# Performance work log

Hardware: AMD Instinct MI355X
Metric: run time of the kernel (lower is better)

The kernel has to match this reference:

```python
import math
import jax, jax.numpy as jnp
import numpy as np
from jax import lax

jax.config.update("jax_enable_x64", True)

DECOMP_LEVEL = 5
# Daubechies-5 (db5) decomposition low-pass filter (pywt convention)
_DB5_LO = np.array([0.003335725285001549, -0.012580751999015526, -0.006241490213011705,
                    0.07757149384006515, -0.03224486958502952, -0.24229488706619015,
                    0.13842814590110342, 0.7243085284385744, 0.6038292697974729,
                    0.160102397974125], dtype=np.float64)
_L = _DB5_LO.size
_DB5_HI = _DB5_LO[::-1].copy() * ((-1.0) ** np.arange(_L))  # QMF high-pass
LO = jnp.asarray(_DB5_LO, jnp.float32)
HI = jnp.asarray(_DB5_HI, jnp.float32)
LOR = jnp.asarray(_DB5_LO[::-1].copy(), jnp.float32)
HIR = jnp.asarray(_DB5_HI[::-1].copy(), jnp.float32)


def _an_last(x):
    # orthonormal periodized analysis along last axis: (..., n) -> (..., n/2) x2
    n = x.shape[-1]
    lead = x.shape[:-1]
    xp = jnp.concatenate([x, x[..., : _L - 2]], axis=-1).reshape(-1, 1, n + _L - 2)
    k = jnp.stack([LO, HI])[:, None, :]  # (2,1,L)
    y = lax.conv_general_dilated(xp, k, (2,), "VALID")  # (B,2,n/2)
    y = y.reshape(lead + (2, n // 2))
    return y[..., 0, :], y[..., 1, :]


def _syn_last(a, d):
    # exact transpose/inverse of _an_last (orthonormal -> W^T = W^-1)
    n2 = a.shape[-1]
    n = 2 * n2
    lead = a.shape[:-1]
    B = int(np.prod(lead)) if lead else 1
    u = jnp.zeros((B, 2, n), a.dtype)
    u = u.at[:, 0, ::2].set(a.reshape(B, n2))
    u = u.at[:, 1, ::2].set(d.reshape(B, n2))
    up = jnp.concatenate([u[..., -(_L - 1):], u], axis=-1)  # circular left pad
    k = jnp.stack([LOR, HIR])[None, :, :]  # (1,2,L)
    y = lax.conv_general_dilated(up, k, (1,), "VALID")  # (B,1,n)
    return y.reshape(lead + (n,))


def _dwt2(x):  # x: (C,h,w) -> ll, lh, hl, hh each (C,h/2,w/2)
    a_h, d_h = _an_last(x.swapaxes(-1, -2))
    a_h = a_h.swapaxes(-1, -2)
    d_h = d_h.swapaxes(-1, -2)
    ll, lh = _an_last(a_h)
    hl, hh = _an_last(d_h)
    return ll, lh, hl, hh


def _idwt2(ll, lh, hl, hh):
    a_h = _syn_last(ll, lh)
    d_h = _syn_last(hl, hh)
    return _syn_last(a_h.swapaxes(-1, -2), d_h.swapaxes(-1, -2)).swapaxes(-1, -2)


def _estimate_noise(data):
    p = data.shape[0]
    rr = data @ data.T
    rri = jnp.linalg.inv(rr + 1e-6 * jnp.eye(p, dtype=data.dtype))
    def per_band(i):
        xx = rri - jnp.outer(rri[:, i], rri[i, :]) / rri[i, i]
        beta = xx @ rr[:, i]
        return beta.at[i].set(0.0)
    betas = jax.vmap(per_band)(jnp.arange(p))  # (p,p)
    return data - betas @ data


def hyres_forward(x):
    H, W, K = x.shape
    N = H * W
    data = x.reshape(N, K).T.astype(jnp.float64)
    w = _estimate_noise(data)
    omega1 = (jnp.sqrt(jnp.var(w, axis=1, ddof=1)) + 1e-30) ** 2  # (K,) f64
    y_w = x * omega1 ** -0.5  # whitened, f64
    u, s, v_pca = jnp.linalg.svd(y_w.reshape(N, K), full_matrices=False)
    pc = (u * s).reshape(W, H, K).astype(jnp.float32).transpose(2, 0, 1)  # (K,H,W)
    # multi-level 2D DWT per channel
    ll = pc
    highs = []
    for _ in range(DECOMP_LEVEL):
        ll, lh, hl, hh = _dwt2(ll)
        highs.append((lh, hl, hh))
    # overwrite-style full coefficient image [[LL,LH],[HL,HH]] recursively
    full = ll
    for lh, hl, hh in reversed(highs):
        top = jnp.concatenate([full, lh], axis=-1)
        bot = jnp.concatenate([hl, hh], axis=-1)
        full = jnp.concatenate([top, bot], axis=-2)
    V = full.transpose(1, 2, 0).reshape(N, K)
    V2 = V * V
    norm_v = jnp.sum(V2)
    n_xyz = jnp.asarray(V.size, jnp.float32)
    col_norm = jnp.sum(V2, axis=0)  # (K,)
    # SURE of soft-threshold over a 15-point grid in [0, sqrt(log N)]
    ts = np.linspace(0.0, math.sqrt(math.log(N)), 15).astype(np.float32)
    sure_cols = []
    for t in ts:
        t2 = float(t * t)
        s_t = (jnp.sum(jnp.minimum(V2, t2), axis=0)
               + 2.0 * jnp.sum((V2 > t2).astype(jnp.float32), axis=0)
               - col_norm)
        sure_cols.append(s_t)
    sure_all = jnp.stack(sure_cols, axis=1)  # (K,15)
    c_const = norm_v - n_xyz
    # replicate the in-place cumulative update: S_r = sum_{j<r} S_j + sure_r + C
    def step(acc, sure_r):
        s_r = acc + sure_r + c_const
        return acc + s_r, jnp.min(s_r)
    _, min_sure = lax.scan(step, jnp.zeros((15,), jnp.float32), sure_all)
    # early-exit: first rank>1 where min_sure increases; else loop ends at K-1
    cond = min_sure[2:] > min_sure[1:-1]
    rank = jnp.where(jnp.any(cond), 2 + jnp.argmax(cond), K - 1)
    mask = (jnp.arange(K) < rank).astype(jnp.float32)[:, None, None]
    # truncation-to-rank == zeroing channels >= rank (inverse DWT is linear)
    y = ll * mask
    for lh, hl, hh in reversed(highs):
        y = _idwt2(y, lh * mask, hl * mask, hh * mask)
    y_est = y.transpose(1, 2, 0).reshape(N, K)  # zero cols beyond rank
    out = (omega1.astype(jnp.float32) ** 0.5) * (y_est @ v_pca.astype(jnp.float32)).reshape(H, W, K)
    return out


def setup_inputs() -> dict:
    key = jax.random.key(0)
    k1, k2, k3 = jax.random.split(key, 3)
    H = W = 384
    K = 191
    R = 8  # low-rank spectral structure + noise, as HyRes assumes
    a = jax.random.normal(k1, (H * W, R), jnp.float32)
    b = jax.random.normal(k2, (R, K), jnp.float32)
    x = (a @ b) / np.sqrt(R) + 0.1 * jax.random.normal(k3, (H * W, K), jnp.float32)
    return {"x": x.reshape(H, W, K)}


def reference(x):
    return hyres_forward(x)
```

## Files before the change

### kernel.cpp

```cpp
#include <hip/hip_runtime.h>
#include <math.h>

#define K_     191
#define LD     192
#define N_     147456
#define MSUB   16
#define NT     15
#define TRI_N  18336
#define SMEM_CHOL  ((TRI_N + 1056 + 64) * 8)
#define SMEM_SOLVE ((TRI_N + 192 + 192 + 192) * 8)
#define SMEM2_SZ (6880 * 8 + 32 * 4 + TRI_N * 4)

#define NPAIR  6
#define NSPLIT 256
#define CHUNK  (N_ / NSPLIT)
#define RSTEP  16

__constant__ float c_lo[10] = {
  0.003335725285001549f, -0.012580751999015526f, -0.006241490213011705f,
  0.07757149384006515f,  -0.03224486958502952f, -0.24229488706619015f,
  0.13842814590110342f,   0.7243085284385744f,   0.6038292697974729f,
  0.160102397974125f };
__constant__ float c_hi[10] = {
  0.160102397974125f,    -0.6038292697974729f,   0.7243085284385744f,
 -0.13842814590110342f,  -0.24229488706619015f,  0.03224486958502952f,
  0.07757149384006515f,   0.006241490213011705f,-0.012580751999015526f,
 -0.003335725285001549f };

__global__ __launch_bounds__(256, 6) void k_rr(const float* __restrict__ x,
                                               double* __restrict__ rrg,
                                               double* __restrict__ m)
{
  __shared__ float Asf[2][RSTEP][64];
  __shared__ float Bsf[2][RSTEP][64];

  const int bid   = blockIdx.x;
  const int split = bid & (NSPLIT - 1);
  const int pair  = bid >> 8;
  const int BI[6] = {0, 0, 0, 1, 1, 2};
  const int BJ[6] = {0, 1, 2, 1, 2, 2};
  const int bi = BI[pair], bj = BJ[pair];
  const int diag = (bi == bj);
  const int ca = bi * 64, cb = bj * 64;

  const int t  = threadIdx.x;
  const int tx = t & 15, ty = t >> 4;
  const int mycol = t & 63, rowgrp = t >> 6;
  const long n0 = (long)split * CHUNK;

  double acc[4][4];
  #pragma unroll
  for (int v = 0; v < 4; ++v)
    #pragma unroll
    for (int u = 0; u < 4; ++u) acc[v][u] = 0.0;
  double csum = 0.0;

  float ra[4], rbv[4];
  const int cA = ca + mycol, cB = cb + mycol;
  const bool okA = (cA < K_), okB = (cB < K_);

  auto LOADT = [&](int r0) {
    #pragma unroll
    for (int i = 0; i < 4; ++i) {
      int row = i * 4 + rowgrp;
      long gr = (n0 + r0 + row) * (long)K_;
      float va = okA ? x[gr + cA] : 0.f;
      ra[i] = va;
      if (diag) csum += (double)va;
      else      rbv[i] = okB ? x[gr + cB] : 0.f;
    }
  };
  auto WRITET = [&](int buf) {
    #pragma unroll
    for (int i = 0; i < 4; ++i) {
      int row = i * 4 + rowgrp;
      Asf[buf][row][mycol] = ra[i];
      if (!diag) Bsf[buf][row][mycol] = rbv[i];
    }
  };

  LOADT(0);
  WRITET(0);
  __syncthreads();

  int cur = 0;
  for (int r0 = 0; r0 < CHUNK; r0 += RSTEP) {
    const bool hasnext = (r0 + RSTEP < CHUNK);
    if (hasnext) LOADT(r0 + RSTEP);
    const float (*As)[64] = Asf[cur];
    const float (*Bs)[64] = diag ? Asf[cur] : Bsf[cur];
    #pragma unroll 4
    for (int k = 0; k < RSTEP; ++k) {
      double a0 = (double)As[k][ty],      a1 = (double)As[k][ty + 16];
      double a2 = (double)As[k][ty + 32], a3 = (double)As[k][ty + 48];
      double b0 = (double)Bs[k][tx],      b1 = (double)Bs[k][tx + 16];
      double b2 = (double)Bs[k][tx + 32], b3 = (double)Bs[k][tx + 48];
      acc[0][0] += a0 * b0; acc[0][1] += a0 * b1; acc[0][2] += a0 * b2; acc[0][3] += a0 * b3;
      acc[1][0] += a1 * b0; acc[1][1] += a1 * b1; acc[1][2] += a1 * b2; acc[1][3] += a1 * b3;
      acc[2][0] += a2 * b0; acc[2][1] += a2 * b1; acc[2][2] += a2 * b2; acc[2][3] += a2 * b3;
      acc[3][0] += a3 * b0; acc[3][1] += a3 * b1; acc[3][2] += a3 * b2; acc[3][3] += a3 * b3;
    }
    if (hasnext) WRITET(cur ^ 1);
    __syncthreads();
    cur ^= 1;
  }

  #pragma unroll
  for (int v = 0; v < 4; ++v) {
    int mrow = ca + ty + 16 * v;
    #pragma unroll
    for (int u = 0; u < 4; ++u) {
      int ncol = cb + tx + 16 * u;
      if (mrow < K_ && ncol < K_ && (!diag || mrow <= ncol))
        atomicAdd(&rrg[(size_t)mrow * K_ + ncol], acc[v][u]);
    }
  }

  if (diag) {
    double* sc = (double*)Bsf;
    sc[t] = csum;
    __syncthreads();
    if (t < 64) {
      int c = ca + t;
      if (c < K_) {
        double s = sc[t] + sc[t + 64] + sc[t + 128] + sc[t + 192];
        atomicAdd(&m[c], s);
      }
    }
  }
}

__global__ __launch_bounds__(256) void k_reduce(const double* __restrict__ rrg,
                                                double* __restrict__ rr)
{
  int idx = blockIdx.x * 256 + threadIdx.x;
  if (idx >= TRI_N) return;
  int i = (int)((sqrtf(8.f * (float)idx + 1.f) - 1.f) * 0.5f);
  while ((i + 1) * (i + 2) / 2 <= idx) ++i;
  while (i * (i + 1) / 2 > idx) --i;
  int j = idx - (i * (i + 1)) / 2;
  double s = rrg[(size_t)j * K_ + i];
  rr[i * LD + j] = s;
  rr[j * LD + i] = s;
}

__global__ __launch_bounds__(512) void k_chol(
    const double* __restrict__ rr, double* __restrict__ Lg,
    double* __restrict__ rdg)
{
  extern __shared__ double smem[];
  double* tri  = smem;
  double* tmp  = smem + TRI_N;
  double* tmp2 = tmp + 1056;
  const int t = threadIdx.x;

  for (int i = t >> 5; i < K_; i += 16) {
    int base = (i * (i + 1)) / 2;
    for (int j = t & 31; j <= i; j += 32) {
      double v = rr[i * LD + j];
      tri[base + j] = (i == j) ? v + 1e-6 : v;
    }
  }
  __syncthreads();

  for (int J = 0; J < 6; ++J) {
    const int j0 = J * 32;
    const int nb = (K_ - j0 < 32) ? (K_ - j0) : 32;

    if (t < 64) {
      const int rl = t & 31;
      double a[32];
      #pragma unroll
      for (int c = 0; c < 32; ++c) {
        int i = j0 + rl;
        a[c] = (c <= rl && rl < nb) ? tri[(i * (i + 1)) / 2 + j0 + c] : 0.0;
      }
      #pragma unroll
      for (int k = 0; k < 32; ++k) {
        double akk = __shfl(a[k], k);
        double piv = sqrt(akk);
        double inv = 1.0 / piv;
        if (t == k) {
          tmp2[k] = inv;
          if (j0 + k < K_) rdg[j0 + k] = inv;
        }
        a[k] = (rl == k) ? piv : a[k] * inv;
        #pragma unroll
        for (int c = k + 1; c < 32; ++c) {
          double lck = __shfl(a[k], c);
          if (c <= rl) a[c] -= a[k] * lck;
        }
      }
      if (t < 32 && rl < nb) {
        int i = j0 + rl;
        int rb = (i * (i + 1)) / 2 + j0;
        #pragma unroll
        for (int c = 0; c < 32; ++c)
          if (c <= rl) tri[rb + c] = a[c];
      }
    }
    if (t < 32) {
      const int c = t;
      double xcol[32];
      #pragma unroll
      for (int r = 0; r < 32; ++r) {
        int rr_ = (j0 + r < K_) ? j0 + r : K_ - 1;
        int rb2 = (rr_ * (rr_ + 1)) / 2 + j0;
        double s = (r == c) ? 1.0 : 0.0;
        #pragma unroll
        for (int k = 0; k < 32; ++k)
          if (k < r) s -= tri[rb2 + k] * xcol[k];
        xcol[r] = s * tmp2[r];
      }
      #pragma unroll
      for (int r = 0; r < 32; ++r)
        tmp[r * 33 + c] = (r >= c) ? xcol[r] : 0.0;
    }
    __syncthreads();

    {
      int p = j0 + 32 + t;
      if (nb == 32 && p < K_) {
        int pb = (p * (p + 1)) / 2 + j0;
        double arow[32];
        #pragma unroll
        for (int k = 0; k < 32; ++k) arow[k] = tri[pb + k];
        #pragma unroll
        for (int c = 0; c < 32; ++c) {
          double s = 0.0;
          #pragma unroll
          for (int k = 0; k < 32; ++k)
            if (k <= c) s += arow[k] * tmp[c * 33 + k];
          tri[pb + c] = s;
        }
      }
    }
    __syncthreads();

    {
      int s0 = j0 + 32;
      int n = K_ - s0;
      if (n > 0) {
        int R4 = (n + 3) >> 2;
        int T4 = R4 * (R4 + 1) / 2;
        for (int tile = t; tile < T4; tile += 512) {
          int ti = (int)((sqrtf(8.f * (float)tile + 1.f) - 1.f) * 0.5f);
          while ((ti + 1) * (ti + 2) / 2 <= tile) ++ti;
          while (ti * (ti + 1) / 2 > tile) --ti;
          int tj = tile - ti * (ti + 1) / 2;
          int r0 = s0 + ti * 4, c0 = s0 + tj * 4;
          int rb[4], cb[4];
          #pragma unroll
          for (int u = 0; u < 4; ++u) {
            int r = (r0 + u < K_) ? r0 + u : K_ - 1;
            rb[u] = (r * (r + 1)) / 2;
            int c = (c0 + u < K_) ? c0 + u : K_ - 1;
            cb[u] = (c * (c + 1)) / 2;
          }
          double acc[4][4];
          #pragma unroll
          for (int u = 0; u < 4; ++u)
            #pragma unroll
            for (int v2 = 0; v2 < 4; ++v2) acc[u][v2] = 0.0;
          #pragma unroll 4
          for (int p = 0; p < 32; ++p) {
            double lr[4], lc[4];
            #pragma unroll
            for (int u = 0; u < 4; ++u) {
              lr[u] = tri[rb[u] + j0 + p];
              lc[u] = tri[cb[u] + j0 + p];
            }
            #pragma unroll
            for (int u = 0; u < 4; ++u)
              #pragma unroll
              for (int v2 = 0; v2 < 4; ++v2) acc[u][v2] += lr[u] * lc[v2];
          }
          #pragma unroll
          for (int u = 0; u < 4; ++u) {
            int r = r0 + u;
            if (r < K_) {
              #pragma unroll
              for (int v2 = 0; v2 < 4; ++v2) {
                int c = c0 + v2;
                if (c <= r) tri[rb[u] + c] -= acc[u][v2];
              }
            }
          }
        }
      }
    }
    __syncthreads();
  }

  for (int idx = t; idx < TRI_N; idx += 512) Lg[idx] = tri[idx];
}

__global__ __launch_bounds__(256) void k_csolve(
    const double* __restrict__ Lg, const double* __restrict__ rdg,
    const double* __restrict__ mg, double* __restrict__ s2g,
    double* __restrict__ zg)
{
  extern __shared__ double ssm[];
  double* Ls   = ssm;
  double* rd_s = Ls + TRI_N;
  double* m_sh = rd_s + 192;
  double* ys   = m_sh + 192;
  const int t = threadIdx.x;
  const int bid = blockIdx.x;

  const int start = (bid < K_) ? (bid * (bid + 1)) / 2 : 0;
  for (int idx = start + t; idx < TRI_N; idx += 256) Ls[idx] = Lg[idx];
  if (t < K_) { rd_s[t] = rdg[t]; m_sh[t] = mg[t]; }
  __syncthreads();

  if (t >= 64) return;
  const int l = t;

  if (bid < K_) {
    const int i = bid;
    double x0 = 0.0, x1 = 0.0, x2 = 0.0;
    {
      double rdi = rd_s[i];
      if ((i & 63) == l) {
        int sl = i >> 6;
        if (sl == 0) x0 = rdi; else if (sl == 1) x1 = rdi; else x2 = rdi;
      }
    }
    for (int r = i + 1; r < K_; ++r) {
      int rb = (r * (r + 1)) >> 1;
      double partial = 0.0;
      { int k = l;       if (k < r) partial += Ls[rb + k] * x0; }
      { int k = l + 64;  if (k < r) partial += Ls[rb + k] * x1; }
      { int k = l + 128; if (k < r) partial += Ls[rb + k] * x2; }
      #pragma unroll
      for (int mm = 32; mm > 0; mm >>= 1) partial += __shfl_xor(partial, mm);
      double val = -partial * rd_s[r];
      if ((r & 63) == l) {
        int sl = r >> 6;
        if (sl == 0) x0 = val; else if (sl == 1) x1 = val; else x2 = val;
      }
    }
    double s2p = x0 * x0 + x1 * x1 + x2 * x2;
    #pragma unroll
    for (int mm = 32; mm > 0; mm >>= 1) s2p += __shfl_xor(s2p, mm);
    if (l == 0) s2g[i] = s2p;
  } else {
    double y0 = 0.0, y1 = 0.0, y2 = 0.0;
    for (int r = 0; r < K_; ++r) {
      int rb = (r * (r + 1)) >> 1;
      double partial = 0.0;
      { int k = l;       if (k < r) partial += Ls[rb + k] * y0; }
      { int k = l + 64;  if (k < r) partial += Ls[rb + k] * y1; }
      { int k = l + 128; if (k < r) partial += Ls[rb + k] * y2; }
      #pragma unroll
      for (int mm = 32; mm > 0; mm >>= 1) partial += __shfl_xor(partial, mm);
      double val = (m_sh[r] - partial) * rd_s[r];
      if ((r & 63) == l) {
        int sl = r >> 6;
        if (sl == 0) y0 = val; else if (sl == 1) y1 = val; else y2 = val;
      }
      if (l == 0) ys[r] = val;
    }
    double z0 = 0.0, z1 = 0.0, z2 = 0.0;
    for (int r = K_ - 1; r >= 0; --r) {
      double partial = 0.0;
      { int k = l;       if (k > r && k < K_) partial += Ls[((k * (k + 1)) >> 1) + r] * z0; }
      { int k = l + 64;  if (k > r && k < K_) partial += Ls[((k * (k + 1)) >> 1) + r] * z1; }
      { int k = l + 128; if (k > r && k < K_) partial += Ls[((k * (k + 1)) >> 1) + r] * z2; }
      #pragma unroll
      for (int mm = 32; mm > 0; mm >>= 1) partial += __shfl_xor(partial, mm);
      double val = (ys[r] - partial) * rd_s[r];
      if ((r & 63) == l) {
        int sl = r >> 6;
        if (sl == 0) z0 = val; else if (sl == 1) z1 = val; else z2 = val;
      }
      if (l == 0) zg[r] = val;
    }
  }
}

__global__ __launch_bounds__(256) void k_finals(
    const double* __restrict__ rr, const double* __restrict__ s2g,
    const double* __restrict__ zg, double* __restrict__ invsq,
    float* __restrict__ normv)
{
  __shared__ double tmps[K_];
  const int t = threadIdx.x;
  if (t < K_) {
    double dii = s2g[t];
    double q = 1.0 / dii;
    double sm_ = zg[t] / dii;
    double var = (q - sm_ * sm_ / (double)N_) / (double)(N_ - 1);
    double t1 = sqrt(var) + 1e-30;
    double om = t1 * t1;
    invsq[t] = 1.0 / sqrt(om);
    tmps[t] = rr[t * LD + t] / om;
  }
  __syncthreads();
  if (t < 64) {
    double s = 0.0;
    for (int i = t; i < K_; i += 64) s += tmps[i];
    #pragma unroll
    for (int off = 32; off > 0; off >>= 1) s += __shfl_down(s, off);
    if (t == 0) *normv = (float)s;
  }
}

__device__ __forceinline__ void cholqr(double* shQ, double* shS, int t)
{
  if (t < MSUB * MSUB) {
    int a = t & (MSUB - 1), b = t >> 4;
    double s = 0.0;
    for (int r = 0; r < K_; ++r) s += shQ[r * MSUB + a] * shQ[r * MSUB + b];
    shS[b * 17 + a] = s;
  }
  __syncthreads();
  for (int k = 0; k < MSUB; ++k) {
    if (t == 0) shS[k * 17 + k] = sqrt(shS[k * 17 + k]);
    __syncthreads();
    if (t > k && t < MSUB) shS[t * 17 + k] /= shS[k * 17 + k];
    __syncthreads();
    if (t < MSUB * MSUB) {
      int r = t & (MSUB - 1), c = t >> 4;
      if (c > k && r >= c) shS[r * 17 + c] -= shS[r * 17 + k] * shS[c * 17 + k];
    }
    __syncthreads();
  }
  if (t < K_) {
    double q[MSUB];
    #pragma unroll
    for (int c = 0; c < MSUB; ++c) {
      double v = shQ[t * MSUB + c];
      for (int p = 0; p < c; ++p) v -= q[p] * shS[c * 17 + p];
      q[c] = v / shS[c * 17 + c];
    }
    #pragma unroll
    for (int c = 0; c < MSUB; ++c) shQ[t * MSUB + c] = q[c];
  }
  __syncthreads();
}

__global__ __launch_bounds__(512) void k_sub(
    const double* __restrict__ rr, const double* __restrict__ invsq,
    float* __restrict__ W1, float* __restrict__ W2)
{
  extern __shared__ double dsm[];
  double* shQ  = dsm;
  double* shZ  = shQ + 3056;
  double* shS  = shZ + 3056;
  double* Ws   = shS + 272;
  double* inv_s= Ws + 272;
  double* ev   = inv_s + 192;
  double* cs_  = ev + 16;
  double* sn_  = cs_ + 8;
  int* ipp  = (int*)(sn_ + 8);
  int* iqq  = ipp + 8;
  int* perm = iqq + 8;
  float* tri = (float*)(perm + 16);
  const int t = threadIdx.x;

  if (t < K_) inv_s[t] = invsq[t];
  __syncthreads();
  for (int i = t >> 4; i < K_; i += 32) {
    int base = (i * (i + 1)) / 2;
    double di = inv_s[i];
    for (int j = t & 15; j <= i; j += 16)
      tri[base + j] = (float)(rr[i * LD + j] * di * inv_s[j]);
  }
  __syncthreads();

  for (int idx = t; idx < K_ * MSUB; idx += 512) {
    int i = idx >> 4, c = idx & 15;
    float g = (i >= c) ? tri[(i * (i + 1)) / 2 + c] : tri[(c * (c + 1)) / 2 + i];
    shQ[idx] = (double)g;
  }
  __syncthreads();

  cholqr(shQ, shS, t);
  for (int it = 0; it < 4; ++it) {
    for (int idx = t; idx < K_ * MSUB; idx += 512) shZ[idx] = shQ[idx];
    __syncthreads();
    if (t < 96 * 4) {
      int i2 = t >> 2, c4 = t & 3;
      int r0 = 2 * i2, r1 = r0 + 1;
      int has1 = (r1 < K_);
      int rb0 = (r0 * (r0 + 1)) >> 1;
      int rb1 = has1 ? ((r1 * (r1 + 1)) >> 1) : rb0;
      int cb0 = c4 * 4;
      double s0a = 0.0, s0b = 0.0, s0c = 0.0, s0d = 0.0;
      double s1a = 0.0, s1b = 0.0, s1c = 0.0, s1d = 0.0;
      #pragma unroll 2
      for (int k = 0; k <= r0; ++k) {
        double g0 = (double)tri[rb0 + k];
        double g1 = (double)tri[rb1 + k];
        double za = shZ[k * MSUB + cb0],     zb = shZ[k * MSUB + cb0 + 1];
        double zc = shZ[k * MSUB + cb0 + 2], zd = shZ[k * MSUB + cb0 + 3];
        s0a += g0 * za; s0b += g0 * zb; s0c += g0 * zc; s0d += g0 * zd;
        s1a += g1 * za; s1b += g1 * zb; s1c += g1 * zc; s1d += g1 * zd;
      }
      if (has1) {
        double g0 = (double)tri[rb1 + r0];
        double g1 = (double)tri[rb1 + r1];
        double za = shZ[r1 * MSUB + cb0],     zb = shZ[r1 * MSUB + cb0 + 1];
        double zc = shZ[r1 * MSUB + cb0 + 2], zd = shZ[r1 * MSUB + cb0 + 3];
        s0a += g0 * za; s0b += g0 * zb; s0c += g0 * zc; s0d += g0 * zd;
        s1a += g1 * za; s1b += g1 * zb; s1c += g1 * zc; s1d += g1 * zd;
      }
      int kk = ((r1 + 1) * (r1 + 2)) >> 1;
      #pragma unroll 2
      for (int k = r1 + 1; k < K_; ++k) {
        double g0 = (double)tri[kk + r0];
        double g1 = (double)tri[kk + r1];
        double za = shZ[k * MSUB + cb0],     zb = shZ[k * MSUB + cb0 + 1];
        double zc = shZ[k * MSUB + cb0 + 2], zd = shZ[k * MSUB + cb0 + 3];
        s0a += g0 * za; s0b += g0 * zb; s0c += g0 * zc; s0d += g0 * zd;
        s1a += g1 * za; s1b += g1 * zb; s1c += g1 * zc; s1d += g1 * zd;
        kk += k + 1;
      }
      shQ[r0 * MSUB + cb0]     = s0a;
      shQ[r0 * MSUB + cb0 + 1] = s0b;
      shQ[r0 * MSUB + cb0 + 2] = s0c;
      shQ[r0 * MSUB + cb0 + 3] = s0d;
      if (has1) {
        shQ[r1 * MSUB + cb0]     = s1a;
        shQ[r1 * MSUB + cb0 + 1] = s1b;
        shQ[r1 * MSUB + cb0 + 2] = s1c;
        shQ[r1 * MSUB + cb0 + 3] = s1d;
      }
    }
    __syncthreads();
    if (it < 3) cholqr(shQ, shS, t);
  }
  if (t < MSUB * MSUB) {
    int a = t & 15, b = t >> 4;
    double s = 0.0;
    for (int r = 0; r < K_; ++r) s += shZ[r * MSUB + b] * shQ[r * MSUB + a];
    shS[b * 17 + a] = s;
  }
  if (t < MSUB * 17) Ws[t] = 0.0;
  __syncthreads();
  if (t < MSUB) Ws[t * 17 + t] = 1.0;
  __syncthreads();
  for (int sweep = 0; sweep < 6; ++sweep) {
    for (int round = 0; round < 15; ++round) {
      if (t < 8) {
        int ia = (t == 0) ? 0 : (1 + ((t - 1 + round) % 15));
        int ib = 1 + ((14 - t + round) % 15);
        int p = ia < ib ? ia : ib;
        int q = ia < ib ? ib : ia;
        double app = shS[p * 17 + p], aqq = shS[q * 17 + q], apq = shS[p * 17 + q];
        double c = 1.0, s = 0.0;
        if (fabs(apq) > 1e-30 * (fabs(app) + fabs(aqq)) && apq != 0.0) {
          double tau = (aqq - app) / (2.0 * apq);
          double tt = (tau >= 0.0 ? 1.0 : -1.0) / (fabs(tau) + sqrt(1.0 + tau * tau));
          c = 1.0 / sqrt(1.0 + tt * tt); s = tt * c;
        }
        cs_[t] = c; sn_[t] = s; ipp[t] = p; iqq[t] = q;
      }
      __syncthreads();
      if (t < 128) {
        int i = t & 15, mI = t >> 4;
        int p = ipp[mI], q = iqq[mI];
        double c = cs_[mI], s = sn_[mI];
        double u = shS[i * 17 + p], v = shS[i * 17 + q];
        shS[i * 17 + p] = c * u - s * v; shS[i * 17 + q] = s * u + c * v;
        double wu = Ws[i * 17 + p], wv = Ws[i * 17 + q];
        Ws[i * 17 + p] = c * wu - s * wv; Ws[i * 17 + q] = s * wu + c * wv;
      }
      __syncthreads();
      if (t < 128) {
        int j = t & 15, mI = t >> 4;
        int p = ipp[mI], q = iqq[mI];
        double c = cs_[mI], s = sn_[mI];
        double u = shS[p * 17 + j], v = shS[q * 17 + j];
        shS[p * 17 + j] = c * u - s * v; shS[q * 17 + j] = s * u + c * v;
      }
      __syncthreads();
    }
  }
  if (t == 0) {
    for (int i = 0; i < MSUB; ++i) { ev[i] = shS[i * 17 + i]; perm[i] = i; }
    for (int i = 0; i < MSUB; ++i) {
      int best = i;
      for (int j = i + 1; j < MSUB; ++j)
        if (ev[perm[j]] > ev[perm[best]]) best = j;
      int tp = perm[i]; perm[i] = perm[best]; perm[best] = tp;
    }
  }
  __syncthreads();
  for (int idx = t; idx < K_ * MSUB; idx += 512) {
    int i = idx >> 4, c = idx & 15;
    int pc_ = perm[c];
    double e = 0.0;
    #pragma unroll
    for (int p = 0; p < MSUB; ++p) e += shZ[i * MSUB + p] * Ws[p * 17 + pc_];
    W1[i * MSUB + c] = (float)(inv_s[i] * e);
    W2[c * K_ + i]   = (float)(e / inv_s[i]);
  }
}

__global__ __launch_bounds__(256) void k_pc(const float* __restrict__ x,
                                            const float* __restrict__ W1,
                                            float* __restrict__ pc)
{
  __shared__ float xs[32][192];
  __shared__ float w1s[K_ * MSUB];
  int t = threadIdx.x;
  long n0 = (long)blockIdx.x * 32;
  for (int idx = t; idx < K_ * MSUB; idx += 256) w1s[idx] = W1[idx];
  for (int idx = t; idx < 32 * K_; idx += 256) {
    int row = idx / K_, col = idx - row * K_;
    xs[row][col] = x[(n0 + row) * K_ + col];
  }
  __syncthreads();
  int c = t & 15, nl = t >> 4;
  float a0 = 0.f, a1 = 0.f;
  for (int k = 0; k < K_; ++k) {
    float w = w1s[k * MSUB + c];
    a0 += xs[nl][k] * w;
    a1 += xs[nl + 16][k] * w;
  }
  __syncthreads();
  float* ts = &xs[0][0];
  ts[c * 33 + nl]      = a0;
  ts[c * 33 + nl + 16] = a1;
  __syncthreads();
  for (int idx = t; idx < MSUB * 32; idx += 256) {
    int cc = idx >> 5, nn = idx & 31;
    pc[(size_t)cc * N_ + n0 + nn] = ts[cc * 33 + nn];
  }
}

__global__ __launch_bounds__(256) void k_dwt2(const float* __restrict__ in,
                                              float* __restrict__ llout,
                                              float* __restrict__ coef,
                                              int s, long offL, int last,
                                              int ntr)
{
  __shared__ float xin[40][41];
  __shared__ float las[16][41];
  __shared__ float lds_[16][41];
  const int h = s >> 1;
  const int t = threadIdx.x;
  int bid = blockIdx.x;
  int ch = bid / (ntr * ntr);
  int rem = bid - ch * (ntr * ntr);
  int tr = rem / ntr, tc = rem - tr * ntr;
  int rv0 = tr * 16, mc0 = tc * 16;
  const float* cin = in + (long)ch * s * s;

  for (int idx = t; idx < 40 * 40; idx += 256) {
    int i = idx / 40, c = idx - i * 40;
    int gr = (2 * rv0 + i) % s;
    int gc = (2 * mc0 + c) % s;
    xin[i][c] = cin[(long)gr * s + gc];
  }
  __syncthreads();

  for (int idx = t; idx < 16 * 40; idx += 256) {
    int i = idx / 40, c = idx - i * 40;
    float la = 0.f, ld = 0.f;
    #pragma unroll
    for (int l = 0; l < 10; ++l) {
      float v = xin[2 * i + l][c];
      la += c_lo[l] * v; ld += c_hi[l] * v;
    }
    las[i][c] = la; lds_[i][c] = ld;
  }
  __syncthreads();

  {
    int i = t >> 4, j = t & 15;
    int rv = rv0 + i, mc = mc0 + j;
    if (rv < h && mc < h) {
      float ll = 0.f, lh = 0.f, hl = 0.f, hh = 0.f;
      #pragma unroll
      for (int l = 0; l < 10; ++l) {
        float a = las[i][2 * j + l];
        float d = lds_[i][2 * j + l];
        ll += c_lo[l] * a; lh += c_hi[l] * a;
        hl += c_lo[l] * d; hh += c_hi[l] * d;
      }
      float* cslab = coef + (size_t)ch * N_ + offL;
      llout[(size_t)ch * h * h + (long)rv * h + mc] = ll;
      if (last) coef[(size_t)ch * N_ + 147312 + (long)rv * h + mc] = ll;
      cslab[(long)rv * h + mc] = lh;
      cslab[(long)h * h + (long)rv * h + mc] = hl;
      cslab[(long)2 * h * h + (long)rv * h + mc] = hh;
    }
  }
}

__global__ __launch_bounds__(256) void k_stats(const float* __restrict__ coef,
                                               float* __restrict__ stats)
{
  int ch = blockIdx.x;
  int t = threadIdx.x;
  float T2[NT];
  {
    double stop = sqrt(log(147456.0));
    double step = stop / 14.0;
    for (int i = 0; i < NT; ++i) {
      double td = (i == 14) ? stop : (double)i * step;
      float tf = (float)td;
      T2[i] = tf * tf;
    }
  }
  float cn = 0.f, sm[NT], ct[NT];
  #pragma unroll
  for (int i = 0; i < NT; ++i) { sm[i] = 0.f; ct[i] = 0.f; }
  const float* base = coef + (size_t)ch * N_;
  for (int idx = t; idx < N_; idx += 256) {
    float v = base[idx];
    float v2 = v * v;
    cn += v2;
    #pragma unroll
    for (int i = 0; i < NT; ++i) {
      sm[i] += fminf(v2, T2[i]);
      ct[i] += (v2 > T2[i]) ? 1.0f : 0.0f;
    }
  }
  __shared__ float red2[4][32];
  int lane = t & 63, wv = t >> 6;
  for (int a = 0; a < 31; ++a) {
    float val = (a == 0) ? cn : ((a < 16) ? sm[a - 1] : ct[a - 16]);
    #pragma unroll
    for (int off = 32; off > 0; off >>= 1) val += __shfl_down(val, off);
    if (lane == 0) red2[wv][a] = val;
  }
  __syncthreads();
  if (t < 31)
    stats[ch * 31 + t] = red2[0][t] + red2[1][t] + red2[2][t] + red2[3][t];
}

__global__ void k_rank(const float* __restrict__ stats,
                       const float* __restrict__ normv, int* __restrict__ rankp)
{
  if (threadIdx.x != 0 || blockIdx.x != 0) return;
  float c_const = *normv - 28164096.0f;
  float acc[NT];
  for (int i = 0; i < NT; ++i) acc[i] = 0.f;
  float minsure[MSUB];
  for (int r = 0; r < MSUB; ++r) {
    float cn = stats[r * 31 + 0];
    float mn = 3.4e38f;
    for (int i = 0; i < NT; ++i) {
      float sure = stats[r * 31 + 1 + i] + 2.0f * stats[r * 31 + 16 + i] - cn;
      float s_r = acc[i] + sure + c_const;
      acc[i] = acc[i] + s_r;
      if (s_r < mn) mn = s_r;
    }
    minsure[r] = mn;
  }
  int rank = -1;
  for (int r = 2; r < MSUB; ++r) {
    if (minsure[r] > minsure[r - 1]) { rank = r; break; }
  }
  if (rank < 0) rank = MSUB - 1;
  *rankp = rank;
}

__global__ __launch_bounds__(256) void k_out(const float* __restrict__ pc,
                                             const float* __restrict__ W2,
                                             const int* __restrict__ rankp,
                                             float* __restrict__ out)
{
  long gid = (long)blockIdx.x * 256 + threadIdx.x;
  int n = (int)(gid / K_);
  int j = (int)(gid - (long)n * K_);
  int rank = *rankp;
  float acc = 0.f;
  for (int c = 0; c < rank; ++c)
    acc += pc[(size_t)c * N_ + n] * W2[c * K_ + j];
  out[gid] = acc;
}

extern "C" void kernel_launch(void* const* d_in, const int* in_sizes, int n_in,
                              void* d_out, int out_size, void* d_ws, size_t ws_size,
                              hipStream_t stream)
{
  if (n_in < 1 || in_sizes[0] != N_ * K_) return;
  const float* x = (const float*)d_in[0];
  float* out = (float*)d_out;
  (void)out_size;

  char* w = (char*)d_ws;
  size_t off = 0;
  auto alloc = [&](size_t bytes) -> char* {
    char* p = w + off;
    off = (off + bytes + 255) & ~(size_t)255;
    return p;
  };
  double* m_    = (double*)alloc(K_ * 8);
  double* rrp   = (double*)alloc((size_t)K_ * K_ * 8);
  double* rr    = (double*)alloc((size_t)K_ * LD * 8);
  double* Lg    = (double*)alloc((size_t)TRI_N * 8);
  double* rdg   = (double*)alloc(192 * 8);
  double* s2g   = (double*)alloc(192 * 8);
  double* zg    = (double*)alloc(192 * 8);
  double* invsq = (double*)alloc(K_ * 8);
  float*  normv = (float*)alloc(256);
  float*  W1    = (float*)alloc((size_t)K_ * MSUB * 4);
  float*  W2    = (float*)alloc((size_t)MSUB * K_ * 4);
  float*  pc    = (float*)alloc((size_t)MSUB * N_ * 4);
  float*  coef  = (float*)alloc((size_t)MSUB * N_ * 4);
  float*  curA  = (float*)alloc((size_t)MSUB * 192 * 192 * 4);
  float*  curB  = (float*)alloc((size_t)MSUB * 96 * 96 * 4);
  float*  stats = (float*)alloc((size_t)MSUB * 31 * 4);
  int*    rankp = (int*)alloc(256);
  if (off > ws_size) return;

  hipMemsetAsync(m_, 0, K_ * sizeof(double), stream);
  hipMemsetAsync(rrp, 0, (size_t)K_ * K_ * sizeof(double), stream);

  hipFuncSetAttribute(reinterpret_cast<const void*>(k_chol),
                      hipFuncAttributeMaxDynamicSharedMemorySize, SMEM_CHOL);
  hipFuncSetAttribute(reinterpret_cast<const void*>(k_csolve),
                      hipFuncAttributeMaxDynamicSharedMemorySize, SMEM_SOLVE);
  hipFuncSetAttribute(reinterpret_cast<const void*>(k_sub),
                      hipFuncAttributeMaxDynamicSharedMemorySize, SMEM2_SZ);

  k_rr<<<NPAIR * NSPLIT, 256, 0, stream>>>(x, rrp, m_);
  k_reduce<<<(TRI_N + 255) / 256, 256, 0, stream>>>(rrp, rr);
  k_chol<<<1, 512, SMEM_CHOL, stream>>>(rr, Lg, rdg);
  k_csolve<<<K_ + 1, 256, SMEM_SOLVE, stream>>>(Lg, rdg, m_, s2g, zg);
  k_finals<<<1, 256, 0, stream>>>(rr, s2g, zg, invsq, normv);
  k_sub<<<1, 512, SMEM2_SZ, stream>>>(rr, invsq, W1, W2);
  k_pc<<<N_ / 32, 256, 0, stream>>>(x, W1, pc);

  int   sizes[5] = {384, 192, 96, 48, 24};
  long  offs[5]  = {0, 110592, 138240, 145152, 146880};
  float* lls[5]  = {curA, curB, curA, curB, curA};
  const float* curin = pc;
  for (int lev = 0; lev < 5; ++lev) {
    int s = sizes[lev], h = s >> 1;
    int ntr = (h + 15) / 16;
    k_dwt2<<<16 * ntr * ntr, 256, 0, stream>>>(curin, lls[lev], coef,
                                               s, offs[lev],
                                               lev == 4 ? 1 : 0, ntr);
    curin = lls[lev];
  }

  k_stats<<<MSUB, 256, 0, stream>>>(coef, stats);
  k_rank<<<1, 64, 0, stream>>>(stats, normv, rankp);
  k_out<<<(N_ * K_) / 256, 256, 0, stream>>>(pc, W2, rankp, out);
}
```

Before: 1.462 ms.

## Split single-block Cholesky into per-panel factor and multi-block trailing update kernels

Replaces the single-workgroup shared-memory blocked Cholesky with a host-driven loop of small kernels that work on a global packed triangle. Each of the 6 panels gets a one-block factor/TRSM kernel, followed by a multi-block kernel for the trailing SYRK update, so the update runs on more compute units. The packed matrix with its diagonal shift is now written directly by the reduce kernel. In exchange the code adds about 11 kernel launches, and all operands now go through global memory/L2 instead of LDS.

```diff
diff --git a/kernel.cpp b/kernel.cpp
--- a/kernel.cpp
+++ b/kernel.cpp
@@ -7,7 +7,6 @@
 #define MSUB   16
 #define NT     15
 #define TRI_N  18336
-#define SMEM_CHOL  ((TRI_N + 1056 + 64) * 8)
 #define SMEM_SOLVE ((TRI_N + 192 + 192 + 192) * 8)
 #define SMEM2_SZ (6880 * 8 + 32 * 4 + TRI_N * 4)
 
@@ -131,7 +130,8 @@
 }
 
 __global__ __launch_bounds__(256) void k_reduce(const double* __restrict__ rrg,
-                                                double* __restrict__ rr)
+                                                double* __restrict__ rr,
+                                                double* __restrict__ Tg)
 {
   int idx = blockIdx.x * 256 + threadIdx.x;
   if (idx >= TRI_N) return;
@@ -142,61 +142,52 @@
   double s = rrg[(size_t)j * K_ + i];
   rr[i * LD + j] = s;
   rr[j * LD + i] = s;
-}
-
-__global__ __launch_bounds__(512) void k_chol(
-    const double* __restrict__ rr, double* __restrict__ Lg,
-    double* __restrict__ rdg)
-{
-  extern __shared__ double smem[];
-  double* tri  = smem;
-  double* tmp  = smem + TRI_N;
-  double* tmp2 = tmp + 1056;
+  Tg[idx] = (i == j) ? s + 1e-6 : s;
+}
+
+__global__ __launch_bounds__(256) void k_pfac(double* __restrict__ Tg,
+                                              double* __restrict__ rdg,
+                                              int j0, int nb)
+{
+  __shared__ double tmpL[32 * 33];
+  __shared__ double tmp[32 * 33];
+  __shared__ double tmp2[32];
   const int t = threadIdx.x;
 
-  for (int i = t >> 5; i < K_; i += 16) {
-    int base = (i * (i + 1)) / 2;
-    for (int j = t & 31; j <= i; j += 32) {
-      double v = rr[i * LD + j];
-      tri[base + j] = (i == j) ? v + 1e-6 : v;
-    }
-  }
-  __syncthreads();
-
-  for (int J = 0; J < 6; ++J) {
-    const int j0 = J * 32;
-    const int nb = (K_ - j0 < 32) ? (K_ - j0) : 32;
-
-    if (t < 64) {
-      const int rl = t & 31;
-      double a[32];
-      #pragma unroll
-      for (int c = 0; c < 32; ++c) {
-        int i = j0 + rl;
-        a[c] = (c <= rl && rl < nb) ? tri[(i * (i + 1)) / 2 + j0 + c] : 0.0;
-      }
-      #pragma unroll
-      for (int k = 0; k < 32; ++k) {
-        double akk = __shfl(a[k], k);
-        double piv = sqrt(akk);
-        double inv = 1.0 / piv;
-        if (t == k) {
-          tmp2[k] = inv;
-          if (j0 + k < K_) rdg[j0 + k] = inv;
-        }
-        a[k] = (rl == k) ? piv : a[k] * inv;
-        #pragma unroll
-        for (int c = k + 1; c < 32; ++c) {
-          double lck = __shfl(a[k], c);
-          if (c <= rl) a[c] -= a[k] * lck;
-        }
-      }
-      if (t < 32 && rl < nb) {
+  if (t < 64) {
+    const int rl = t & 31;
+    double a[32];
+    #pragma unroll
+    for (int c = 0; c < 32; ++c) {
+      int i = j0 + rl;
+      a[c] = (c <= rl && rl < nb) ? Tg[(i * (i + 1)) / 2 + j0 + c] : 0.0;
+    }
+    #pragma unroll
+    for (int k = 0; k < 32; ++k) {
+      double akk = __shfl(a[k], k);
+      double piv = sqrt(akk);
+      double inv = 1.0 / piv;
+      if (t == k) {
+        tmp2[k] = inv;
+        if (j0 + k < K_) rdg[j0 + k] = inv;
+      }
+      a[k] = (rl == k) ? piv : a[k] * inv;
+      #pragma unroll
+      for (int c = k + 1; c < 32; ++c) {
+        double lck = __shfl(a[k], c);
+        if (c <= rl) a[c] -= a[k] * lck;
+      }
+    }
+    if (t < 32) {
+      #pragma unroll
+      for (int c = 0; c < 32; ++c)
+        if (c <= rl) tmpL[rl * 33 + c] = a[c];
+      if (rl < nb) {
         int i = j0 + rl;
         int rb = (i * (i + 1)) / 2 + j0;
         #pragma unroll
         for (int c = 0; c < 32; ++c)
-          if (c <= rl) tri[rb + c] = a[c];
+          if (c <= rl) Tg[rb + c] = a[c];
       }
     }
     if (t < 32) {
@@ -204,95 +195,88 @@
       double xcol[32];
       #pragma unroll
       for (int r = 0; r < 32; ++r) {
-        int rr_ = (j0 + r < K_) ? j0 + r : K_ - 1;
-        int rb2 = (rr_ * (rr_ + 1)) / 2 + j0;
         double s = (r == c) ? 1.0 : 0.0;
         #pragma unroll
         for (int k = 0; k < 32; ++k)
-          if (k < r) s -= tri[rb2 + k] * xcol[k];
+          if (k < r) s -= tmpL[r * 33 + k] * xcol[k];
         xcol[r] = s * tmp2[r];
       }
       #pragma unroll
       for (int r = 0; r < 32; ++r)
         tmp[r * 33 + c] = (r >= c) ? xcol[r] : 0.0;
     }
-    __syncthreads();
-
-    {
-      int p = j0 + 32 + t;
-      if (nb == 32 && p < K_) {
-        int pb = (p * (p + 1)) / 2 + j0;
-        double arow[32];
+  }
+  __syncthreads();
+
+  {
+    int p = j0 + 32 + t;
+    if (nb == 32 && p < K_) {
+      int pb = (p * (p + 1)) / 2 + j0;
+      double arow[32];
+      #pragma unroll
+      for (int k = 0; k < 32; ++k) arow[k] = Tg[pb + k];
+      #pragma unroll
+      for (int c = 0; c < 32; ++c) {
+        double s = 0.0;
         #pragma unroll
-        for (int k = 0; k < 32; ++k) arow[k] = tri[pb + k];
-        #pragma unroll
-        for (int c = 0; c < 32; ++c) {
-          double s = 0.0;
-          #pragma unroll
-          for (int k = 0; k < 32; ++k)
-            if (k <= c) s += arow[k] * tmp[c * 33 + k];
-          tri[pb + c] = s;
-        }
-      }
-    }
-    __syncthreads();
-
-    {
-      int s0 = j0 + 32;
-      int n = K_ - s0;
-      if (n > 0) {
-        int R4 = (n + 3) >> 2;
-        int T4 = R4 * (R4 + 1) / 2;
-        for (int tile = t; tile < T4; tile += 512) {
-          int ti = (int)((sqrtf(8.f * (float)tile + 1.f) - 1.f) * 0.5f);
-          while ((ti + 1) * (ti + 2) / 2 <= tile) ++ti;
-          while (ti * (ti + 1) / 2 > tile) --ti;
-          int tj = tile - ti * (ti + 1) / 2;
-          int r0 = s0 + ti * 4, c0 = s0 + tj * 4;
-          int rb[4], cb[4];
-          #pragma unroll
-          for (int u = 0; u < 4; ++u) {
-            int r = (r0 + u < K_) ? r0 + u : K_ - 1;
-            rb[u] = (r * (r + 1)) / 2;
-            int c = (c0 + u < K_) ? c0 + u : K_ - 1;
-            cb[u] = (c * (c + 1)) / 2;
-          }
-          double acc[4][4];
-          #pragma unroll
-          for (int u = 0; u < 4; ++u)
-            #pragma unroll
-            for (int v2 = 0; v2 < 4; ++v2) acc[u][v2] = 0.0;
-          #pragma unroll 4
-          for (int p = 0; p < 32; ++p) {
-            double lr[4], lc[4];
-            #pragma unroll
-            for (int u = 0; u < 4; ++u) {
-              lr[u] = tri[rb[u] + j0 + p];
-              lc[u] = tri[cb[u] + j0 + p];
-            }
-            #pragma unroll
-            for (int u = 0; u < 4; ++u)
-              #pragma unroll
-              for (int v2 = 0; v2 < 4; ++v2) acc[u][v2] += lr[u] * lc[v2];
-          }
-          #pragma unroll
-          for (int u = 0; u < 4; ++u) {
-            int r = r0 + u;
-            if (r < K_) {
-              #pragma unroll
-              for (int v2 = 0; v2 < 4; ++v2) {
-                int c = c0 + v2;
-                if (c <= r) tri[rb[u] + c] -= acc[u][v2];
-              }
-            }
-          }
-        }
-      }
-    }
-    __syncthreads();
-  }
-
-  for (int idx = t; idx < TRI_N; idx += 512) Lg[idx] = tri[idx];
+        for (int k = 0; k < 32; ++k)
+          if (k <= c) s += arow[k] * tmp[c * 33 + k];
+        Tg[pb + c] = s;
+      }
+    }
+  }
+}
+
+__global__ __launch_bounds__(256) void k_ptrail(double* __restrict__ Tg, int j0)
+{
+  const int s0 = j0 + 32;
+  const int n = K_ - s0;
+  const int R4 = (n + 3) >> 2;
+  const int T4 = R4 * (R4 + 1) / 2;
+  int tile = blockIdx.x * 256 + threadIdx.x;
+  if (tile >= T4) return;
+  int ti = (int)((sqrtf(8.f * (float)tile + 1.f) - 1.f) * 0.5f);
+  while ((ti + 1) * (ti + 2) / 2 <= tile) ++ti;
+  while (ti * (ti + 1) / 2 > tile) --ti;
+  int tj = tile - ti * (ti + 1) / 2;
+  int r0 = s0 + ti * 4, c0 = s0 + tj * 4;
+  int rb[4], cb[4];
+  #pragma unroll
+  for (int u = 0; u < 4; ++u) {
+    int r = (r0 + u < K_) ? r0 + u : K_ - 1;
+    rb[u] = (r * (r + 1)) / 2;
+    int c = (c0 + u < K_) ? c0 + u : K_ - 1;
+    cb[u] = (c * (c + 1)) / 2;
+  }
+  double acc[4][4];
+  #pragma unroll
+  for (int u = 0; u < 4; ++u)
+    #pragma unroll
+    for (int v2 = 0; v2 < 4; ++v2) acc[u][v2] = 0.0;
+  #pragma unroll 4
+  for (int p = 0; p < 32; ++p) {
+    double lr[4], lc[4];
+    #pragma unroll
+    for (int u = 0; u < 4; ++u) {
+      lr[u] = Tg[rb[u] + j0 + p];
+      lc[u] = Tg[cb[u] + j0 + p];
+    }
+    #pragma unroll
+    for (int u = 0; u < 4; ++u)
+      #pragma unroll
+      for (int v2 = 0; v2 < 4; ++v2) acc[u][v2] += lr[u] * lc[v2];
+  }
+  #pragma unroll
+  for (int u = 0; u < 4; ++u) {
+    int r = r0 + u;
+    if (r < K_) {
+      #pragma unroll
+      for (int v2 = 0; v2 < 4; ++v2) {
+        int c = c0 + v2;
+        if (c <= r) Tg[rb[u] + c] -= acc[u][v2];
+      }
+    }
+  }
 }
 
 __global__ __launch_bounds__(256) void k_csolve(
@@ -794,7 +778,7 @@
   double* m_    = (double*)alloc(K_ * 8);
   double* rrp   = (double*)alloc((size_t)K_ * K_ * 8);
   double* rr    = (double*)alloc((size_t)K_ * LD * 8);
-  double* Lg    = (double*)alloc((size_t)TRI_N * 8);
+  double* Tg    = (double*)alloc((size_t)TRI_N * 8);
   double* rdg   = (double*)alloc(192 * 8);
   double* s2g   = (double*)alloc(192 * 8);
   double* zg    = (double*)alloc(192 * 8);
@@ -813,17 +797,27 @@
   hipMemsetAsync(m_, 0, K_ * sizeof(double), stream);
   hipMemsetAsync(rrp, 0, (size_t)K_ * K_ * sizeof(double), stream);
 
-  hipFuncSetAttribute(reinterpret_cast<const void*>(k_chol),
-                      hipFuncAttributeMaxDynamicSharedMemorySize, SMEM_CHOL);
   hipFuncSetAttribute(reinterpret_cast<const void*>(k_csolve),
                       hipFuncAttributeMaxDynamicSharedMemorySize, SMEM_SOLVE);
   hipFuncSetAttribute(reinterpret_cast<const void*>(k_sub),
                       hipFuncAttributeMaxDynamicSharedMemorySize, SMEM2_SZ);
 
   k_rr<<<NPAIR * NSPLIT, 256, 0, stream>>>(x, rrp, m_);
-  k_reduce<<<(TRI_N + 255) / 256, 256, 0, stream>>>(rrp, rr);
-  k_chol<<<1, 512, SMEM_CHOL, stream>>>(rr, Lg, rdg);
-  k_csolve<<<K_ + 1, 256, SMEM_SOLVE, stream>>>(Lg, rdg, m_, s2g, zg);
+  k_reduce<<<(TRI_N + 255) / 256, 256, 0, stream>>>(rrp, rr, Tg);
+
+  for (int J = 0; J < 6; ++J) {
+    int j0 = J * 32;
+    int nb = (K_ - j0 < 32) ? (K_ - j0) : 32;
+    k_pfac<<<1, 256, 0, stream>>>(Tg, rdg, j0, nb);
+    int s0 = j0 + 32, n = K_ - s0;
+    if (n > 0) {
+      int R4 = (n + 3) >> 2;
+      int T4 = R4 * (R4 + 1) / 2;
+      k_ptrail<<<(T4 + 255) / 256, 256, 0, stream>>>(Tg, j0);
+    }
+  }
+
+  k_csolve<<<K_ + 1, 256, SMEM_SOLVE, stream>>>(Tg, rdg, m_, s2g, zg);
   k_finals<<<1, 256, 0, stream>>>(rr, s2g, zg, invsq, normv);
   k_sub<<<1, 512, SMEM2_SZ, stream>>>(rr, invsq, W1, W2);
   k_pc<<<N_ / 32, 256, 0, stream>>>(x, W1, pc);
```

After: 1.470 ms. Within noise of the previous version (+0.5%).
